# Performance work log

Hardware: AMD Instinct MI355X
Metric: run time of the kernel (lower is better)

## Reference

```python
import jax, jax.numpy as jnp
import numpy as np

NUM_HEADS = 4
NUM_GROUPS = 8
EPS = 1e-5


def setup_inputs() -> dict:
    key = jax.random.key(0)
    ks = jax.random.split(key, 4)
    B, C, H, W = 4, 256, 64, 64
    x = jax.random.normal(ks[0], (B, C, H, W), dtype=jnp.float32)
    gamma = jnp.ones((C,), dtype=jnp.float32)
    beta = jnp.zeros((C,), dtype=jnp.float32)
    w_qkv = jax.random.normal(ks[1], (3 * C, C), dtype=jnp.float32) * 0.02
    b_qkv = jnp.zeros((3 * C,), dtype=jnp.float32)
    w_proj = jax.random.normal(ks[2], (C, C), dtype=jnp.float32) * 0.02
    b_proj = jnp.zeros((C,), dtype=jnp.float32)
    return {"x": x, "gamma": gamma, "beta": beta, "w_qkv": w_qkv,
            "b_qkv": b_qkv, "w_proj": w_proj, "b_proj": b_proj}


def _group_norm(x, gamma, beta):
    B, C, H, W = x.shape
    xg = x.reshape(B, NUM_GROUPS, C // NUM_GROUPS, H, W)
    mean = xg.mean(axis=(2, 3, 4), keepdims=True)
    var = xg.var(axis=(2, 3, 4), keepdims=True)
    xn = ((xg - mean) * jax.lax.rsqrt(var + EPS)).reshape(B, C, H, W)
    return xn * gamma[None, :, None, None] + beta[None, :, None, None]


def reference(x, gamma, beta, w_qkv, b_qkv, w_proj, b_proj):
    B, C, H, W = x.shape
    d = C // NUM_HEADS
    scale = d ** (-0.5)
    xn = _group_norm(x, gamma, beta)
    # 1x1 conv == per-pixel linear: (B,C,H,W) x (3C,C) -> (B,3C,H,W)
    qkv = jnp.einsum('bchw,oc->bohw', xn, w_qkv) + b_qkv[None, :, None, None]
    q, k, v = jnp.split(qkv, 3, axis=1)
    S = H * W
    q = q.reshape(B, NUM_HEADS, d, S)  # (B,h,d,S)
    k = k.reshape(B, NUM_HEADS, d, S)
    v = v.reshape(B, NUM_HEADS, d, S)
    # attn scores: q^T k, scaled AFTER the matmul (as in source)
    attn = jax.nn.softmax(jnp.einsum('bhds,bhdt->bhst', q, k) * scale, axis=-1)
    # out = attn @ v^T -> (B,h,S,d) then transpose to (B,h,d,S) -> (B,C,H,W)
    out = jnp.einsum('bhst,bhdt->bhds', attn, v).reshape(B, C, H, W)
    y = jnp.einsum('bchw,oc->bohw', out, w_proj) + b_proj[None, :, None, None]
    return x + y
```

## Files before the change

kernel.cpp:

```cpp
#include <hip/hip_runtime.h>
#include <hip/hip_bf16.h>


typedef __attribute__((ext_vector_type(8))) short          b16x8;
typedef __attribute__((ext_vector_type(4))) float          f32x4;
typedef __attribute__((ext_vector_type(4))) unsigned short u16x4;
typedef __attribute__((ext_vector_type(8))) unsigned short u16x8;

#define SWZ(row, chunk) (((chunk) ^ ((row) & 7)))

__device__ __forceinline__ unsigned short f2bf(float f) {
    union { float f; unsigned u; } v; v.f = f;
    unsigned r = v.u + 0x7FFF + ((v.u >> 16) & 1);
    return (unsigned short)(r >> 16);
}

__device__ __forceinline__ float bf2f(unsigned short u) {
    union { unsigned u; float f; } v; v.u = ((unsigned)u) << 16;
    return v.f;
}

__device__ __forceinline__ unsigned bfpack_trunc(float lo, float hi) {
    union { float f; unsigned u; } a, b;
    a.f = hi; b.f = lo;
    return __builtin_amdgcn_perm(a.u, b.u, 0x07060302u);
}

__device__ __forceinline__ float fexp2(float x) {
#if __has_builtin(__builtin_amdgcn_exp2f)
    return __builtin_amdgcn_exp2f(x);
#else
    return exp2f(x);
#endif
}

__device__ __forceinline__ float frcp(float x) {
#if __has_builtin(__builtin_amdgcn_rcpf)
    return __builtin_amdgcn_rcpf(x);
#else
    return 1.f / x;
#endif
}

__device__ __forceinline__ void gll16(const void* g, void* l) {
    __builtin_amdgcn_global_load_lds(
        (const __attribute__((address_space(1))) unsigned int*)g,
        (__attribute__((address_space(3))) unsigned int*)l, 16, 0, 0);
}

__global__ __launch_bounds__(256) void gn_prepack(const float* __restrict__ x,
                                                  float* __restrict__ partials,
                                                  const float* __restrict__ wqkv,
                                                  const float* __restrict__ bqkv,
                                                  unsigned short* __restrict__ wsw,
                                                  float* __restrict__ bq_pre,
                                                  const float* __restrict__ wproj,
                                                  unsigned short* __restrict__ wswp) {
    int bx = blockIdx.x;
    int t = threadIdx.x;
    if (bx < 512) {
        int bg = bx >> 4, part = bx & 15;
        const float* xp = x + (size_t)bg * 131072 + (size_t)part * 8192;
        float s = 0.f, ss = 0.f;
        for (int k = 0; k < 8; k++) {
            float4 v = *(const float4*)(xp + t * 4 + k * 1024);
            s += v.x + v.y + v.z + v.w;
            ss += v.x * v.x + v.y * v.y + v.z * v.z + v.w * v.w;
        }
        for (int off = 32; off; off >>= 1) {
            s += __shfl_down(s, off);
            ss += __shfl_down(ss, off);
        }
        __shared__ float rs[4], rss[4];
        if ((t & 63) == 0) { rs[t >> 6] = s; rss[t >> 6] = ss; }
        __syncthreads();
        if (t == 0) {
            partials[2 * bx]     = rs[0] + rs[1] + rs[2] + rs[3];
            partials[2 * bx + 1] = rss[0] + rss[1] + rss[2] + rss[3];
        }
    } else if (bx < 608) {
        int gid = (bx - 512) * 256 + t;
        const float qs = 0.125f * 1.44269504f;
        int o = gid >> 5, ch = gid & 31, cblk = ch >> 3, chl = ch & 7;
        float sc = (o < 256) ? qs : 1.f;
        const float* src = &wqkv[o * 256 + ch * 8];
        u16x8 v;
        for (int i = 0; i < 8; i++) v[i] = f2bf(src[i] * sc);
        *(u16x8*)&wsw[((cblk * 768 + o) << 6) + SWZ(o, chl) * 8] = v;
        if (gid < 768) bq_pre[gid] = bqkv[gid] * ((gid < 256) ? qs : 1.f);
    } else {
        int gid = (bx - 608) * 256 + t;
        int o = gid >> 5, ch = gid & 31, cblk = ch >> 3, chl = ch & 7;
        const float* src = &wproj[o * 256 + ch * 8];
        u16x8 v;
        for (int i = 0; i < 8; i++) v[i] = f2bf(src[i]);
        *(u16x8*)&wswp[((cblk * 256 + o) << 6) + SWZ(o, chl) * 8] = v;
    }
}

__global__ __launch_bounds__(256) void qkv_gemm(const float* __restrict__ x,
                                                const float* __restrict__ gamma,
                                                const float* __restrict__ beta,
                                                const unsigned short* __restrict__ wsw,
                                                const float* __restrict__ bq_pre,
                                                const float* __restrict__ partials,
                                                unsigned short* __restrict__ qT,
                                                unsigned short* __restrict__ kT,
                                                unsigned short* __restrict__ vT) {
    __shared__ __align__(16) unsigned short Asm[256 * 64];
    __shared__ __align__(16) unsigned short Bsm[64 * 72];
    __shared__ float stats_s[16];
    int s0 = blockIdx.x * 64, sec = blockIdx.y, b = blockIdx.z;
    int t = threadIdx.x, lane = t & 63, wv = t >> 6;
    int l15 = lane & 15, quad = lane >> 4;
    f32x4 acc[4][4] = {};

    if (t < 8) {
        float s = 0.f, ss = 0.f;
        for (int p = 0; p < 16; p++) {
            s  += partials[2 * ((b * 8 + t) * 16 + p)];
            ss += partials[2 * ((b * 8 + t) * 16 + p) + 1];
        }
        const float invN = 1.f / 131072.f;
        float mean = s * invN;
        float var = ss * invN - mean * mean;
        stats_s[2 * t] = mean;
        stats_s[2 * t + 1] = rsqrtf(var + 1e-5f);
    }

    int tc = t >> 5;
    int ts = (t & 31) * 2;

    for (int k0 = 0; k0 < 256; k0 += 64) {
        int cblk = k0 >> 6;
        __syncthreads();
        const unsigned short* asrc = wsw + (((size_t)cblk * 768 + sec * 256) << 6);
        for (int j = 0; j < 8; j++) {
            int blk = wv * 8 + j;
            gll16(asrc + blk * 512 + lane * 8, &Asm[blk * 512]);
        }
        {
            int cbase = k0 + tc * 8;
            int g = cbase >> 5;
            float mean = stats_s[2 * g], rstd = stats_s[2 * g + 1];
            u16x8 r0, r1;
            for (int ci = 0; ci < 8; ci++) {
                int c = cbase + ci;
                float2 xv = *(const float2*)&x[((size_t)(b * 256 + c)) * 4096 + s0 + ts];
                float ga = gamma[c] * rstd, be = beta[c] - mean * gamma[c] * rstd;
                r0[ci] = (short)f2bf(xv.x * ga + be);
                r1[ci] = (short)f2bf(xv.y * ga + be);
            }
            *(u16x8*)&Bsm[(ts + 0) * 72 + tc * 8] = r0;
            *(u16x8*)&Bsm[(ts + 1) * 72 + tc * 8] = r1;
        }
        __syncthreads();
        for (int kc = 0; kc < 2; kc++) {
            b16x8 bb[4];
            for (int nn = 0; nn < 4; nn++)
                bb[nn] = *(const b16x8*)(Bsm + (nn * 16 + l15) * 72 + kc * 32 + quad * 8);
            for (int ot = 0; ot < 4; ot++) {
                int row = wv * 16 + l15;
                b16x8 a = *(const b16x8*)&Asm[(ot * 64 + row) * 64 + SWZ(row, kc * 4 + quad) * 8];
                for (int nn = 0; nn < 4; nn++)
                    acc[ot][nn] = __builtin_amdgcn_mfma_f32_16x16x32_bf16(a, bb[nn], acc[ot][nn], 0, 0, 0);
            }
        }
    }

    if (sec < 2) {
        unsigned short* dstT = (sec == 0) ? qT : kT;
        for (int ot = 0; ot < 4; ot++) {
            __syncthreads();
            for (int nn = 0; nn < 4; nn++) {
                u16x4 pv;
                for (int r = 0; r < 4; r++) {
                    int o = sec * 256 + ot * 64 + wv * 16 + quad * 4 + r;
                    pv[r] = f2bf(acc[ot][nn][r] + bq_pre[o]);
                }
                *(u16x4*)&Bsm[(nn * 16 + l15) * 72 + wv * 16 + quad * 4] = pv;
            }
            __syncthreads();
            unsigned short* dst = dstT + (size_t)(b * 4 + ot) * 4096 * 64;
            int s_l = t >> 2;
            for (int j = 0; j < 2; j++) {
                int cp = (t & 3) * 2 + j;
                u16x8 val = *(u16x8*)&Bsm[s_l * 72 + cp * 8];
                *(u16x8*)&dst[(size_t)(s0 + s_l) * 64 + SWZ(s_l, cp) * 8] = val;
            }
        }
    } else {
        int kt = blockIdx.x;
        for (int ot = 0; ot < 4; ot++) {
            int bh = b * 4 + ot;
            for (int r = 0; r < 4; r++) {
                int dd = wv * 16 + quad * 4 + r;
                float bs = bq_pre[512 + ot * 64 + dd];
                u16x4 pv = { f2bf(acc[ot][0][r] + bs), f2bf(acc[ot][1][r] + bs),
                             f2bf(acc[ot][2][r] + bs), f2bf(acc[ot][3][r] + bs) };
                size_t off = ((size_t)(bh * 64 + kt) * 64 + dd) * 64
                           + SWZ(dd, l15 >> 1) * 8 + (l15 & 1) * 4;
                *(u16x4*)&vT[off] = pv;
            }
        }
    }
}

__global__ __launch_bounds__(128, 2) void attn_kernel(const unsigned short* __restrict__ qT,
                                                      const unsigned short* __restrict__ kT,
                                                      const unsigned short* __restrict__ vT,
                                                      unsigned short* __restrict__ Opart,
                                                      float* __restrict__ lsum) {
    __shared__ __align__(16) unsigned short QP[128 * 64];
    __shared__ __align__(16) unsigned short Ksm[2][64 * 64];
    __shared__ __align__(16) unsigned short Vsm[64 * 64];
    int bx = blockIdx.x;
    int q0 = (bx >> 1) * 128;
    int half = bx & 1;
    int kt0 = half * 32, ktN = kt0 + 32;
    int h = blockIdx.y, b = blockIdx.z;
    int bh = b * 4 + h, slab = bh * 2 + half;
    int t = threadIdx.x, lane = t & 63, wv = t >> 6;
    int l15 = lane & 15, quad = lane >> 4;

    const unsigned short* qTb = qT + (size_t)bh * 4096 * 64;
    const unsigned short* kTb = kT + (size_t)bh * 4096 * 64;
    const unsigned short* vTb = vT + (size_t)bh * 64 * 4096;

    for (int j = 0; j < 16; j++) {
        int i = wv + 2 * j;
        if (i < 16) {
            gll16(qTb + (size_t)q0 * 64 + i * 512 + lane * 8, &QP[i * 512]);
        } else if (i < 24) {
            int ii = i - 16;
            gll16(kTb + (size_t)kt0 * 4096 + ii * 512 + lane * 8, &Ksm[0][ii * 512]);
        } else {
            int ii = i - 24;
            gll16(vTb + (size_t)kt0 * 4096 + ii * 512 + lane * 8, &Vsm[ii * 512]);
        }
    }
    __syncthreads();

    b16x8 aq[4][2];
    for (int mt = 0; mt < 4; mt++)
        for (int kc = 0; kc < 2; kc++) {
            int row = wv * 64 + mt * 16 + l15;
            aq[mt][kc] = *(const b16x8*)&QP[row * 64 + SWZ(row, kc * 4 + quad) * 8];
        }

    b16x8 ones;
    for (int i = 0; i < 8; i++) ones[i] = (short)0x3F80;

    f32x4 O[4][4] = {};
    f32x4 lsacc[4] = {};

    for (int kt = kt0; kt < ktN; kt++) {
        int cur = kt & 1;
        int nb = cur ^ 1;
        u16x8 vpre[4];
        bool more = (kt < ktN - 1);
        if (more) {
            for (int j = 0; j < 4; j++) {
                int blk = wv * 4 + j;
                gll16(kTb + (size_t)(kt + 1) * 4096 + blk * 512 + lane * 8,
                      &Ksm[nb][blk * 512]);
            }
            const unsigned short* vsrc = vTb + (size_t)(kt + 1) * 4096;
            for (int j = 0; j < 4; j++)
                vpre[j] = *(const u16x8*)&vsrc[j * 1024 + t * 8];
        }

        f32x4 sc[4][4] = {};
        for (int kc = 0; kc < 2; kc++) {
            b16x8 bk[4];
            for (int nk = 0; nk < 4; nk++) {
                int row = nk * 16 + l15;
                bk[nk] = *(const b16x8*)&Ksm[cur][row * 64 + SWZ(l15, kc * 4 + quad) * 8];
            }
            for (int mt = 0; mt < 4; mt++)
                for (int nk = 0; nk < 4; nk++)
                    sc[mt][nk] = __builtin_amdgcn_mfma_f32_16x16x32_bf16(
                        aq[mt][kc], bk[nk], sc[mt][nk], 0, 0, 0);
        }

        for (int mt = 0; mt < 4; mt++) {
            for (int r = 0; r < 4; r++) {
                float p0 = fexp2(sc[mt][0][r]);
                float p1 = fexp2(sc[mt][1][r]);
                float p2 = fexp2(sc[mt][2][r]);
                float p3 = fexp2(sc[mt][3][r]);
                int row = wv * 64 + mt * 16 + quad * 4 + r;
                uint2 pk = { bfpack_trunc(p0, p1), bfpack_trunc(p2, p3) };
                *(uint2*)&QP[row * 64 + SWZ(row, l15 >> 1) * 8 + (l15 & 1) * 4] = pk;
            }
        }

        for (int kc = 0; kc < 2; kc++) {
            b16x8 ap[4], bv[4];
            for (int mt = 0; mt < 4; mt++) {
                int row = wv * 64 + mt * 16 + l15;
                ap[mt] = *(const b16x8*)&QP[row * 64 + SWZ(row, kc * 4 + quad) * 8];
            }
            for (int nf = 0; nf < 4; nf++) {
                int row = nf * 16 + l15;
                bv[nf] = *(const b16x8*)&Vsm[row * 64 + SWZ(l15, kc * 4 + quad) * 8];
            }
            for (int mt = 0; mt < 4; mt++) {
                lsacc[mt] = __builtin_amdgcn_mfma_f32_16x16x32_bf16(
                    ap[mt], ones, lsacc[mt], 0, 0, 0);
                for (int nf = 0; nf < 4; nf++)
                    O[mt][nf] = __builtin_amdgcn_mfma_f32_16x16x32_bf16(
                        ap[mt], bv[nf], O[mt][nf], 0, 0, 0);
            }
        }

        __syncthreads();
        if (more) {
            for (int j = 0; j < 4; j++)
                *(u16x8*)&Vsm[j * 1024 + t * 8] = vpre[j];
            __syncthreads();
        }
    }

    for (int mt = 0; mt < 4; mt++)
        for (int r = 0; r < 4; r++) {
            int srow = q0 + wv * 64 + mt * 16 + quad * 4 + r;
            if (l15 == 0) lsum[(size_t)slab * 4096 + srow] = lsacc[mt][r];
        }

    for (int mt = 0; mt < 4; mt++)
        for (int nf = 0; nf < 4; nf++)
            for (int r = 0; r < 4; r++) {
                int s = q0 + wv * 64 + mt * 16 + quad * 4 + r;
                int d = nf * 16 + l15;
                Opart[((size_t)slab * 4096 + s) * 64 + d] = f2bf(O[mt][nf][r]);
            }
}

__global__ __launch_bounds__(256) void proj_gemm(const unsigned short* __restrict__ Opart,
                                                 const float* __restrict__ lsum,
                                                 const unsigned short* __restrict__ wswp,
                                                 const float* __restrict__ bias,
                                                 const float* __restrict__ x,
                                                 float* __restrict__ out) {
    __shared__ __align__(16) unsigned short Asm[64 * 64];
    __shared__ __align__(16) unsigned short Bsm[64 * 72];
    int s0 = blockIdx.x * 64, o0 = blockIdx.y * 64, b = blockIdx.z;
    int t = threadIdx.x, lane = t & 63, wv = t >> 6;
    int l15 = lane & 15, quad = lane >> 4;
    int rl = t >> 2;
    f32x4 acc[4] = {};
    for (int k0 = 0; k0 < 256; k0 += 64) {
        int cblk = k0 >> 6;
        __syncthreads();
        const unsigned short* asrc = wswp + (((size_t)cblk * 256 + o0) << 6);
        for (int j = 0; j < 2; j++) {
            int blk = wv * 2 + j;
            gll16(asrc + blk * 512 + lane * 8, &Asm[blk * 512]);
        }
        {
            int bh = b * 4 + cblk;
            int s = s0 + rl;
            float l0 = lsum[(size_t)(bh * 2 + 0) * 4096 + s];
            float l1 = lsum[(size_t)(bh * 2 + 1) * 4096 + s];
            float rcp = frcp(l0 + l1);
            for (int j = 0; j < 2; j++) {
                int off = (t & 3) * 16 + j * 8;
                u16x8 o0v = *(const u16x8*)&Opart[((size_t)(bh * 2 + 0) * 4096 + s) * 64 + off];
                u16x8 o1v = *(const u16x8*)&Opart[((size_t)(bh * 2 + 1) * 4096 + s) * 64 + off];
                u16x8 res;
                for (int i = 0; i < 8; i++)
                    res[i] = f2bf((bf2f(o0v[i]) + bf2f(o1v[i])) * rcp);
                *(u16x8*)&Bsm[rl * 72 + off] = res;
            }
        }
        __syncthreads();
        for (int kc = 0; kc < 2; kc++) {
            int row = wv * 16 + l15;
            b16x8 a = *(const b16x8*)&Asm[row * 64 + SWZ(row, kc * 4 + quad) * 8];
            for (int nn = 0; nn < 4; nn++) {
                b16x8 bb = *(const b16x8*)(Bsm + (nn * 16 + l15) * 72 + kc * 32 + quad * 8);
                acc[nn] = __builtin_amdgcn_mfma_f32_16x16x32_bf16(a, bb, acc[nn], 0, 0, 0);
            }
        }
    }
    for (int nn = 0; nn < 4; nn++) {
        for (int r = 0; r < 4; r++) {
            int o = o0 + wv * 16 + quad * 4 + r;
            int s = s0 + nn * 16 + l15;
            size_t idx = ((size_t)(b * 256 + o)) * 4096 + s;
            out[idx] = acc[nn][r] + bias[o] + x[idx];
        }
    }
}

extern "C" void kernel_launch(void* const* d_in, const int* in_sizes, int n_in,
                              void* d_out, int out_size, void* d_ws, size_t ws_size,
                              hipStream_t stream) {
    const float* x      = (const float*)d_in[0];
    const float* gamma  = (const float*)d_in[1];
    const float* beta   = (const float*)d_in[2];
    const float* w_qkv  = (const float*)d_in[3];
    const float* b_qkv  = (const float*)d_in[4];
    const float* w_proj = (const float*)d_in[5];
    const float* b_proj = (const float*)d_in[6];
    float* out = (float*)d_out;

    unsigned short* ws = (unsigned short*)d_ws;
    unsigned short* qT    = ws;
    unsigned short* kT    = qT + (size_t)16 * 4096 * 64;
    unsigned short* vT    = kT + (size_t)16 * 4096 * 64;
    unsigned short* scratch = vT + (size_t)16 * 4096 * 64;
    unsigned short* Opart = scratch + (size_t)4 * 4096 * 256;
    float*          lsump = (float*)(Opart + (size_t)32 * 4096 * 64);
    unsigned short* wqkv_sw = (unsigned short*)lsump;
    float*          bq_pre  = (float*)((char*)lsump + 393216);
    float*          partials = (float*)scratch;
    unsigned short* wproj_sw = scratch + 32768;

    hipLaunchKernelGGL(gn_prepack,  dim3(640),      dim3(256), 0, stream,
                       x, partials, w_qkv, b_qkv, wqkv_sw, bq_pre, w_proj, wproj_sw);
    hipLaunchKernelGGL(qkv_gemm,    dim3(64, 3, 4), dim3(256), 0, stream,
                       x, gamma, beta, wqkv_sw, bq_pre, partials, qT, kT, vT);
    hipLaunchKernelGGL(attn_kernel, dim3(64, 4, 4), dim3(128), 0, stream,
                       qT, kT, vT, Opart, lsump);
    hipLaunchKernelGGL(proj_gemm,   dim3(64, 4, 4), dim3(256), 0, stream,
                       Opart, lsump, wproj_sw, b_proj, x, out);
}
```

Baseline: 183.0 us.

## Split attention softmax/PV into halves, drop ones-MFMA rowsum, direct QK stores

The attention inner loop now computes the score tile in two column halves and interleaves exp/pack of one half with the PV MFMAs of the other, so transcendental work can overlap matrix work. The row-sum of probabilities is accumulated in fp32 registers and reduced once with shuffles at the end, replacing a per-iteration MFMA against a ones vector. The QKV GEMM epilogue writes Q/K straight to global memory in the swizzled layout instead of staging through shared memory with two barriers, and the V stores use packed 32-bit writes. The costs are smaller, less coalesced global stores in the epilogue, and a rowsum taken from fp32 values instead of the bf16-rounded probabilities used by PV, which slightly changes the normalization.

After: 233.3 us. +27.5%, slower.

```diff
diff --git a/kernel.cpp b/kernel.cpp
--- a/kernel.cpp
+++ b/kernel.cpp
@@ -170,23 +170,15 @@
 
     if (sec < 2) {
         unsigned short* dstT = (sec == 0) ? qT : kT;
+        int ddbase = wv * 16 + quad * 4;
         for (int ot = 0; ot < 4; ot++) {
-            __syncthreads();
+            unsigned short* dst = dstT + (size_t)(b * 4 + ot) * 4096 * 64;
             for (int nn = 0; nn < 4; nn++) {
+                int s = s0 + nn * 16 + l15;
                 u16x4 pv;
-                for (int r = 0; r < 4; r++) {
-                    int o = sec * 256 + ot * 64 + wv * 16 + quad * 4 + r;
-                    pv[r] = f2bf(acc[ot][nn][r] + bq_pre[o]);
-                }
-                *(u16x4*)&Bsm[(nn * 16 + l15) * 72 + wv * 16 + quad * 4] = pv;
-            }
-            __syncthreads();
-            unsigned short* dst = dstT + (size_t)(b * 4 + ot) * 4096 * 64;
-            int s_l = t >> 2;
-            for (int j = 0; j < 2; j++) {
-                int cp = (t & 3) * 2 + j;
-                u16x8 val = *(u16x8*)&Bsm[s_l * 72 + cp * 8];
-                *(u16x8*)&dst[(size_t)(s0 + s_l) * 64 + SWZ(s_l, cp) * 8] = val;
+                for (int r = 0; r < 4; r++)
+                    pv[r] = f2bf(acc[ot][nn][r] + bq_pre[sec * 256 + ot * 64 + ddbase + r]);
+                *(u16x4*)&dst[(size_t)s * 64 + SWZ(s, ddbase >> 3) * 8 + (ddbase & 7)] = pv;
             }
         }
     } else {
@@ -196,11 +188,11 @@
             for (int r = 0; r < 4; r++) {
                 int dd = wv * 16 + quad * 4 + r;
                 float bs = bq_pre[512 + ot * 64 + dd];
-                u16x4 pv = { f2bf(acc[ot][0][r] + bs), f2bf(acc[ot][1][r] + bs),
-                             f2bf(acc[ot][2][r] + bs), f2bf(acc[ot][3][r] + bs) };
-                size_t off = ((size_t)(bh * 64 + kt) * 64 + dd) * 64
-                           + SWZ(dd, l15 >> 1) * 8 + (l15 & 1) * 4;
-                *(u16x4*)&vT[off] = pv;
+                unsigned w01 = bfpack_trunc(acc[ot][0][r] + bs, acc[ot][1][r] + bs);
+                unsigned w23 = bfpack_trunc(acc[ot][2][r] + bs, acc[ot][3][r] + bs);
+                size_t base = ((size_t)(bh * 64 + kt) * 64 + dd) * 64;
+                *(unsigned*)&vT[base + SWZ(dd, l15 >> 2) * 8 + ((l15 * 2) & 7)]       = w01;
+                *(unsigned*)&vT[base + SWZ(dd, 4 + (l15 >> 2)) * 8 + ((l15 * 2) & 7)] = w23;
             }
         }
     }
@@ -248,11 +240,8 @@
             aq[mt][kc] = *(const b16x8*)&QP[row * 64 + SWZ(row, kc * 4 + quad) * 8];
         }
 
-    b16x8 ones;
-    for (int i = 0; i < 8; i++) ones[i] = (short)0x3F80;
-
     f32x4 O[4][4] = {};
-    f32x4 lsacc[4] = {};
+    float ls[4][4] = {};
 
     for (int kt = kt0; kt < ktN; kt++) {
         int cur = kt & 1;
@@ -272,46 +261,72 @@
 
         f32x4 sc[4][4] = {};
         for (int kc = 0; kc < 2; kc++) {
-            b16x8 bk[4];
-            for (int nk = 0; nk < 4; nk++) {
-                int row = nk * 16 + l15;
-                bk[nk] = *(const b16x8*)&Ksm[cur][row * 64 + SWZ(l15, kc * 4 + quad) * 8];
-            }
-            for (int mt = 0; mt < 4; mt++)
-                for (int nk = 0; nk < 4; nk++)
-                    sc[mt][nk] = __builtin_amdgcn_mfma_f32_16x16x32_bf16(
-                        aq[mt][kc], bk[nk], sc[mt][nk], 0, 0, 0);
-        }
-
-        for (int mt = 0; mt < 4; mt++) {
+            b16x8 bk0 = *(const b16x8*)&Ksm[cur][(0 * 16 + l15) * 64 + SWZ(l15, kc * 4 + quad) * 8];
+            b16x8 bk1 = *(const b16x8*)&Ksm[cur][(1 * 16 + l15) * 64 + SWZ(l15, kc * 4 + quad) * 8];
+            for (int mt = 0; mt < 4; mt++) {
+                sc[mt][0] = __builtin_amdgcn_mfma_f32_16x16x32_bf16(aq[mt][kc], bk0, sc[mt][0], 0, 0, 0);
+                sc[mt][1] = __builtin_amdgcn_mfma_f32_16x16x32_bf16(aq[mt][kc], bk1, sc[mt][1], 0, 0, 0);
+            }
+        }
+        for (int kc = 0; kc < 2; kc++) {
+            b16x8 bk2 = *(const b16x8*)&Ksm[cur][(2 * 16 + l15) * 64 + SWZ(l15, kc * 4 + quad) * 8];
+            b16x8 bk3 = *(const b16x8*)&Ksm[cur][(3 * 16 + l15) * 64 + SWZ(l15, kc * 4 + quad) * 8];
+            for (int mt = 0; mt < 4; mt++) {
+                sc[mt][2] = __builtin_amdgcn_mfma_f32_16x16x32_bf16(aq[mt][kc], bk2, sc[mt][2], 0, 0, 0);
+                sc[mt][3] = __builtin_amdgcn_mfma_f32_16x16x32_bf16(aq[mt][kc], bk3, sc[mt][3], 0, 0, 0);
+            }
+        }
+
+        for (int mt = 0; mt < 4; mt++)
             for (int r = 0; r < 4; r++) {
                 float p0 = fexp2(sc[mt][0][r]);
                 float p1 = fexp2(sc[mt][1][r]);
-                float p2 = fexp2(sc[mt][2][r]);
-                float p3 = fexp2(sc[mt][3][r]);
+                ls[mt][r] += p0 + p1;
                 int row = wv * 64 + mt * 16 + quad * 4 + r;
-                uint2 pk = { bfpack_trunc(p0, p1), bfpack_trunc(p2, p3) };
-                *(uint2*)&QP[row * 64 + SWZ(row, l15 >> 1) * 8 + (l15 & 1) * 4] = pk;
-            }
-        }
-
-        for (int kc = 0; kc < 2; kc++) {
+                *(unsigned*)&QP[row * 64 + SWZ(row, l15 >> 2) * 8 + ((l15 * 2) & 7)] =
+                    bfpack_trunc(p0, p1);
+            }
+
+        for (int kc = 0; kc < 1; kc++) {
             b16x8 ap[4], bv[4];
             for (int mt = 0; mt < 4; mt++) {
                 int row = wv * 64 + mt * 16 + l15;
-                ap[mt] = *(const b16x8*)&QP[row * 64 + SWZ(row, kc * 4 + quad) * 8];
+                ap[mt] = *(const b16x8*)&QP[row * 64 + SWZ(row, quad) * 8];
             }
             for (int nf = 0; nf < 4; nf++) {
                 int row = nf * 16 + l15;
-                bv[nf] = *(const b16x8*)&Vsm[row * 64 + SWZ(l15, kc * 4 + quad) * 8];
-            }
-            for (int mt = 0; mt < 4; mt++) {
-                lsacc[mt] = __builtin_amdgcn_mfma_f32_16x16x32_bf16(
-                    ap[mt], ones, lsacc[mt], 0, 0, 0);
+                bv[nf] = *(const b16x8*)&Vsm[row * 64 + SWZ(row, quad) * 8];
+            }
+            for (int mt = 0; mt < 4; mt++)
                 for (int nf = 0; nf < 4; nf++)
                     O[mt][nf] = __builtin_amdgcn_mfma_f32_16x16x32_bf16(
                         ap[mt], bv[nf], O[mt][nf], 0, 0, 0);
-            }
+        }
+
+        for (int mt = 0; mt < 4; mt++)
+            for (int r = 0; r < 4; r++) {
+                float p2 = fexp2(sc[mt][2][r]);
+                float p3 = fexp2(sc[mt][3][r]);
+                ls[mt][r] += p2 + p3;
+                int row = wv * 64 + mt * 16 + quad * 4 + r;
+                *(unsigned*)&QP[row * 64 + SWZ(row, 4 + (l15 >> 2)) * 8 + ((l15 * 2) & 7)] =
+                    bfpack_trunc(p2, p3);
+            }
+
+        {
+            b16x8 ap[4], bv[4];
+            for (int mt = 0; mt < 4; mt++) {
+                int row = wv * 64 + mt * 16 + l15;
+                ap[mt] = *(const b16x8*)&QP[row * 64 + SWZ(row, 4 + quad) * 8];
+            }
+            for (int nf = 0; nf < 4; nf++) {
+                int row = nf * 16 + l15;
+                bv[nf] = *(const b16x8*)&Vsm[row * 64 + SWZ(row, 4 + quad) * 8];
+            }
+            for (int mt = 0; mt < 4; mt++)
+                for (int nf = 0; nf < 4; nf++)
+                    O[mt][nf] = __builtin_amdgcn_mfma_f32_16x16x32_bf16(
+                        ap[mt], bv[nf], O[mt][nf], 0, 0, 0);
         }
 
         __syncthreads();
@@ -324,8 +339,10 @@
 
     for (int mt = 0; mt < 4; mt++)
         for (int r = 0; r < 4; r++) {
+            float s = ls[mt][r];
+            for (int off = 1; off < 16; off <<= 1) s += __shfl_xor(s, off);
             int srow = q0 + wv * 64 + mt * 16 + quad * 4 + r;
-            if (l15 == 0) lsum[(size_t)slab * 4096 + srow] = lsacc[mt][r];
+            if (l15 == 0) lsum[(size_t)slab * 4096 + srow] = s;
         }
 
     for (int mt = 0; mt < 4; mt++)
```

## Drop LDS staging for V and qkv stores; compute row sums with adds

Applied to the files above, without the earlier changes.

The qkv projection epilogue now writes q/k tiles straight to global memory in swizzled layout, removing the LDS staging buffer and two barriers per output tile. The attention kernel drops the V shared-memory buffer and its register prefetch, reading V fragments directly from global/L2 inside the PV loop. It also replaces the ones-vector MFMA row sum with scalar fp32 accumulation plus a cross-lane shuffle reduction. This frees LDS and cuts barriers and MFMA work, at the cost of exposing global-load latency on the V reads and making the stores less coalesced.

New measurement: 181.6 us. No clear change (-0.7%).

```diff
diff --git a/kernel.cpp b/kernel.cpp
--- a/kernel.cpp
+++ b/kernel.cpp
@@ -170,23 +170,15 @@
 
     if (sec < 2) {
         unsigned short* dstT = (sec == 0) ? qT : kT;
+        int ddbase = wv * 16 + quad * 4;
         for (int ot = 0; ot < 4; ot++) {
-            __syncthreads();
+            unsigned short* dst = dstT + (size_t)(b * 4 + ot) * 4096 * 64;
             for (int nn = 0; nn < 4; nn++) {
+                int s = s0 + nn * 16 + l15;
                 u16x4 pv;
-                for (int r = 0; r < 4; r++) {
-                    int o = sec * 256 + ot * 64 + wv * 16 + quad * 4 + r;
-                    pv[r] = f2bf(acc[ot][nn][r] + bq_pre[o]);
-                }
-                *(u16x4*)&Bsm[(nn * 16 + l15) * 72 + wv * 16 + quad * 4] = pv;
-            }
-            __syncthreads();
-            unsigned short* dst = dstT + (size_t)(b * 4 + ot) * 4096 * 64;
-            int s_l = t >> 2;
-            for (int j = 0; j < 2; j++) {
-                int cp = (t & 3) * 2 + j;
-                u16x8 val = *(u16x8*)&Bsm[s_l * 72 + cp * 8];
-                *(u16x8*)&dst[(size_t)(s0 + s_l) * 64 + SWZ(s_l, cp) * 8] = val;
+                for (int r = 0; r < 4; r++)
+                    pv[r] = f2bf(acc[ot][nn][r] + bq_pre[sec * 256 + ot * 64 + ddbase + r]);
+                *(u16x4*)&dst[(size_t)s * 64 + SWZ(s, ddbase >> 3) * 8 + (ddbase & 7)] = pv;
             }
         }
     } else {
@@ -213,7 +205,6 @@
                                                       float* __restrict__ lsum) {
     __shared__ __align__(16) unsigned short QP[128 * 64];
     __shared__ __align__(16) unsigned short Ksm[2][64 * 64];
-    __shared__ __align__(16) unsigned short Vsm[64 * 64];
     int bx = blockIdx.x;
     int q0 = (bx >> 1) * 128;
     int half = bx & 1;
@@ -227,16 +218,13 @@
     const unsigned short* kTb = kT + (size_t)bh * 4096 * 64;
     const unsigned short* vTb = vT + (size_t)bh * 64 * 4096;
 
-    for (int j = 0; j < 16; j++) {
+    for (int j = 0; j < 12; j++) {
         int i = wv + 2 * j;
         if (i < 16) {
             gll16(qTb + (size_t)q0 * 64 + i * 512 + lane * 8, &QP[i * 512]);
-        } else if (i < 24) {
+        } else {
             int ii = i - 16;
             gll16(kTb + (size_t)kt0 * 4096 + ii * 512 + lane * 8, &Ksm[0][ii * 512]);
-        } else {
-            int ii = i - 24;
-            gll16(vTb + (size_t)kt0 * 4096 + ii * 512 + lane * 8, &Vsm[ii * 512]);
         }
     }
     __syncthreads();
@@ -248,16 +236,12 @@
             aq[mt][kc] = *(const b16x8*)&QP[row * 64 + SWZ(row, kc * 4 + quad) * 8];
         }
 
-    b16x8 ones;
-    for (int i = 0; i < 8; i++) ones[i] = (short)0x3F80;
-
     f32x4 O[4][4] = {};
-    f32x4 lsacc[4] = {};
+    float ls[4][4] = {};
 
     for (int kt = kt0; kt < ktN; kt++) {
         int cur = kt & 1;
         int nb = cur ^ 1;
-        u16x8 vpre[4];
         bool more = (kt < ktN - 1);
         if (more) {
             for (int j = 0; j < 4; j++) {
@@ -265,9 +249,6 @@
                 gll16(kTb + (size_t)(kt + 1) * 4096 + blk * 512 + lane * 8,
                       &Ksm[nb][blk * 512]);
             }
-            const unsigned short* vsrc = vTb + (size_t)(kt + 1) * 4096;
-            for (int j = 0; j < 4; j++)
-                vpre[j] = *(const u16x8*)&vsrc[j * 1024 + t * 8];
         }
 
         f32x4 sc[4][4] = {};
@@ -289,9 +270,14 @@
                 float p1 = fexp2(sc[mt][1][r]);
                 float p2 = fexp2(sc[mt][2][r]);
                 float p3 = fexp2(sc[mt][3][r]);
+                ls[mt][r] += (p0 + p1) + (p2 + p3);
                 int row = wv * 64 + mt * 16 + quad * 4 + r;
-                uint2 pk = { bfpack_trunc(p0, p1), bfpack_trunc(p2, p3) };
-                *(uint2*)&QP[row * 64 + SWZ(row, l15 >> 1) * 8 + (l15 & 1) * 4] = pk;
+                u16x4 pk;
+                pk[0] = (unsigned short)(bfpack_trunc(p0, p1) & 0xFFFF);
+                union { unsigned u[2]; u16x4 v; } pku;
+                pku.u[0] = bfpack_trunc(p0, p1);
+                pku.u[1] = bfpack_trunc(p2, p3);
+                *(u16x4*)&QP[row * 64 + SWZ(row, l15 >> 1) * 8 + (l15 & 1) * 4] = pku.v;
             }
         }
 
@@ -303,29 +289,24 @@
             }
             for (int nf = 0; nf < 4; nf++) {
                 int row = nf * 16 + l15;
-                bv[nf] = *(const b16x8*)&Vsm[row * 64 + SWZ(l15, kc * 4 + quad) * 8];
-            }
-            for (int mt = 0; mt < 4; mt++) {
-                lsacc[mt] = __builtin_amdgcn_mfma_f32_16x16x32_bf16(
-                    ap[mt], ones, lsacc[mt], 0, 0, 0);
+                bv[nf] = *(const b16x8*)&vTb[(size_t)kt * 4096 + row * 64
+                                             + SWZ(l15, kc * 4 + quad) * 8];
+            }
+            for (int mt = 0; mt < 4; mt++)
                 for (int nf = 0; nf < 4; nf++)
                     O[mt][nf] = __builtin_amdgcn_mfma_f32_16x16x32_bf16(
                         ap[mt], bv[nf], O[mt][nf], 0, 0, 0);
-            }
-        }
-
-        __syncthreads();
-        if (more) {
-            for (int j = 0; j < 4; j++)
-                *(u16x8*)&Vsm[j * 1024 + t * 8] = vpre[j];
-            __syncthreads();
-        }
+        }
+
+        __syncthreads();
     }
 
     for (int mt = 0; mt < 4; mt++)
         for (int r = 0; r < 4; r++) {
+            float s = ls[mt][r];
+            for (int off = 1; off < 16; off <<= 1) s += __shfl_xor(s, off);
             int srow = q0 + wv * 64 + mt * 16 + quad * 4 + r;
-            if (l15 == 0) lsum[(size_t)slab * 4096 + srow] = lsacc[mt][r];
+            if (l15 == 0) lsum[(size_t)slab * 4096 + srow] = s;
         }
 
     for (int mt = 0; mt < 4; mt++)
```
